# Optimization experiments

Measured on AMD Instinct MI355X. Metric: run time of the kernel, lower is better.

Reference implementation:

```python
import jax, jax.numpy as jnp
import numpy as np

N = 1024
NODE_DIM = 3
HIDDEN = 128
NLAYERS = 3
HEADS = 4
HD = HIDDEN // HEADS  # 32
EPS = 1e-5
NEG = -1e9


def setup_inputs() -> dict:
    key = jax.random.key(0)
    ks = jax.random.split(key, 32)
    def w(k, shape, fan_in):
        return jax.random.normal(k, shape, jnp.float32) / np.sqrt(fan_in).astype(np.float32)
    node_features = jax.random.normal(ks[0], (N, NODE_DIM), jnp.float32)
    adj = jax.random.randint(ks[1], (N, N), 0, 2).astype(jnp.float32)
    adj = adj.at[jnp.arange(N), jnp.arange(N)].set(1.0)  # self-loops
    inp = dict(
        node_features=node_features,
        adj=adj,
        Wp=w(ks[2], (NODE_DIM, HIDDEN), NODE_DIM), bp=jnp.zeros((HIDDEN,), jnp.float32),
        Wl=w(ks[3], (NLAYERS, HIDDEN, HIDDEN), HIDDEN),
        Wr=w(ks[4], (NLAYERS, HIDDEN, HIDDEN), HIDDEN),
        Wv=w(ks[5], (NLAYERS, HIDDEN, HIDDEN), HIDDEN),
        att=w(ks[6], (NLAYERS, HD), HD),
        gamma=jnp.ones((NLAYERS, HIDDEN), jnp.float32),
        beta=jnp.zeros((NLAYERS, HIDDEN), jnp.float32),
        Wn1=w(ks[7], (HIDDEN, 64), HIDDEN), bn1=jnp.zeros((64,), jnp.float32),
        Wn2=w(ks[8], (64, 1), 64), bn2=jnp.zeros((1,), jnp.float32),
        Wd1=w(ks[9], (HIDDEN, 64), HIDDEN), bd1=jnp.zeros((64,), jnp.float32),
        Wd2=w(ks[10], (64, 2), 64), bd2=jnp.zeros((2,), jnp.float32),
        Wv1=w(ks[11], (HIDDEN, 64), HIDDEN), bv1=jnp.zeros((64,), jnp.float32),
        Wv2=w(ks[12], (64, 1), 64), bv2=jnp.zeros((1,), jnp.float32),
    )
    return inp


def _gat_layer(h, mask, Wl, Wr, Wv, att, gamma, beta):
    n = h.shape[0]
    wlh = (h @ Wl).reshape(n, HEADS, HD)
    wrh = (h @ Wr).reshape(n, HEADS, HD)
    # pair[i,j,h,d] = LeakyReLU(Wl h_i + Wr h_j)  -- the O(N^2 H D) tensor
    pair = jax.nn.leaky_relu(wlh[:, None, :, :] + wrh[None, :, :, :], 0.2)
    e = jnp.einsum('ijhd,d->ijh', pair, att)
    e = jnp.where(mask[:, :, None], e, NEG)
    alpha = jax.nn.softmax(e, axis=1)  # softmax over neighbours j (dropout = identity in eval)
    v = (h @ Wv).reshape(n, HEADS, HD)
    agg = jnp.einsum('ijh,jhd->ihd', alpha, v).reshape(n, HIDDEN)
    mu = agg.mean(-1, keepdims=True)
    var = agg.var(-1, keepdims=True)
    out = (agg - mu) / jnp.sqrt(var + EPS) * gamma + beta
    return jax.nn.relu(out)


def reference(node_features, adj, Wp, bp, Wl, Wr, Wv, att, gamma, beta,
              Wn1, bn1, Wn2, bn2, Wd1, bd1, Wd2, bd2, Wv1, bv1, Wv2, bv2):
    mask = adj > 0.5
    h = jax.nn.relu(node_features @ Wp + bp)
    for l in range(NLAYERS):
        h = h + _gat_layer(h, mask, Wl[l], Wr[l], Wv[l], att[l], gamma[l], beta[l])
    node_logits = (jax.nn.relu(h @ Wn1 + bn1) @ Wn2 + bn2).squeeze(-1)
    delta_mu = jax.nn.relu(h @ Wd1 + bd1) @ Wd2 + bd2
    pooled = h.mean(axis=0)
    value = (jax.nn.relu(pooled @ Wv1 + bv1) @ Wv2 + bv2).squeeze(-1)
    return (node_logits, delta_mu, value)
```

## Files before the change

### kernel.cpp

```cpp
#include <hip/hip_runtime.h>
#include <hip/hip_bf16.h>

#define NN 1024
#define HID 128
#define NHEADS 4
#define HDD 32
#define NL 3

constexpr int OFF_CONV = 16;
constexpr int OFF_NF   = OFF_CONV;
constexpr int OFF_WP   = OFF_NF  + 3072;
constexpr int OFF_BP   = OFF_WP  + 384;
constexpr int OFF_WL   = OFF_BP  + 128;
constexpr int OFF_WR   = OFF_WL  + 49152;
constexpr int OFF_WVW  = OFF_WR  + 49152;
constexpr int OFF_ATT  = OFF_WVW + 49152;
constexpr int OFF_GAM  = OFF_ATT + 96;
constexpr int OFF_BET  = OFF_GAM + 384;
constexpr int OFF_WN1  = OFF_BET + 384;
constexpr int OFF_BN1  = OFF_WN1 + 8192;
constexpr int OFF_WN2  = OFF_BN1 + 64;
constexpr int OFF_BN2  = OFF_WN2 + 64;
constexpr int OFF_WD1  = OFF_BN2 + 1;
constexpr int OFF_BD1  = OFF_WD1 + 8192;
constexpr int OFF_WD2  = OFF_BD1 + 64;
constexpr int OFF_BD2  = OFF_WD2 + 128;
constexpr int OFF_WV1  = OFF_BD2 + 2;
constexpr int OFF_BV1  = OFF_WV1 + 8192;
constexpr int OFF_WV2  = OFF_BV1 + 64;
constexpr int OFF_BV2  = OFF_WV2 + 64;
constexpr int OFF_CONV_END = OFF_BV2 + 1;
constexpr int CONV_TOTAL = OFF_CONV_END - OFF_CONV;
constexpr int CB = (CONV_TOTAL + 255) / 256;
constexpr int OFF_MASK = 176960;
constexpr int OFF_H    = OFF_MASK + NN*32;
constexpr int OFF_WLH  = OFF_H   + NN*HID;
constexpr int OFF_WRH  = OFF_WLH + NN*HID;
constexpr int OFF_WVH  = OFF_WRH + NN*HID;
constexpr int OFF_CL   = OFF_WVH + NN*HID;
constexpr int OFF_CR   = OFF_CL  + NHEADS*NN;

__device__ __forceinline__ float bf2f(unsigned short u) {
    return __uint_as_float(((unsigned)u) << 16);
}
__device__ __forceinline__ void store_out(void* out, int idx, float v, bool bf) {
    if (bf) {
        unsigned u = __float_as_uint(v);
        unsigned r = (u + 0x7FFFu + ((u >> 16) & 1u)) >> 16;
        ((unsigned short*)out)[idx] = (unsigned short)r;
    } else {
        ((float*)out)[idx] = v;
    }
}
__device__ __forceinline__ float ldraw(const void* p, int idx, bool bf) {
    return bf ? bf2f(((const unsigned short*)p)[idx]) : ((const float*)p)[idx];
}
__device__ __forceinline__ bool detect_bf(const unsigned* nf) {
    unsigned w = nf[threadIdx.x & 63];
    int e = (int)((w >> 23) & 0xFFu);
    unsigned long long b = __ballot(e >= 110 && e <= 140);
    return __popcll(b) < 32;
}

struct P21 { const void* p[21]; };
__device__ const int g_sizes[21] = {3072,384,128,49152,49152,49152,96,384,384,
                                    8192,64,64,1,8192,64,128,2,8192,64,64,1};
__device__ const int g_dsts[21] = {OFF_NF,OFF_WP,OFF_BP,OFF_WL,OFF_WR,OFF_WVW,OFF_ATT,
                                   OFF_GAM,OFF_BET,OFF_WN1,OFF_BN1,OFF_WN2,OFF_BN2,
                                   OFF_WD1,OFF_BD1,OFF_WD2,OFF_BD2,OFF_WV1,OFF_BV1,
                                   OFF_WV2,OFF_BV2};

__global__ __launch_bounds__(256) void k_pre(P21 in, const void* adj, const unsigned* nf, float* ws) {
    bool bf = detect_bf(nf);
    int b = blockIdx.x, t = threadIdx.x;
    if (b < CB) {
        int g = b * 256 + t;
        if (g >= CONV_TOTAL) return;
        int rem = g, s = 0;
        while (s < 21 && rem >= g_sizes[s]) { rem -= g_sizes[s]; s++; }
        if (s >= 21) return;
        ws[g_dsts[s] + rem] = ldraw(in.p[s], rem, bf);
    } else if (b < CB + NN) {
        int i = b - CB;
        unsigned* mask = (unsigned*)(ws + OFF_MASK);
        int lane = t & 63, wv = t >> 6;
        #pragma unroll
        for (int q = 0; q < 4; q++) {
            int seg = wv * 4 + q;
            int j = seg * 64 + lane;
            float v = ldraw(adj, i * NN + j, bf);
            unsigned long long bl = __ballot(v > 0.5f);
            if (lane == 0) {
                mask[i * 32 + seg * 2]     = (unsigned)bl;
                mask[i * 32 + seg * 2 + 1] = (unsigned)(bl >> 32);
            }
        }
    } else {
        int bb = b - CB - NN;
        int i = bb * 2 + (t >> 7), c = t & 127;
        float a = ldraw(in.p[2], c, bf);
        #pragma unroll
        for (int k = 0; k < 3; k++)
            a += ldraw(in.p[0], i * 3 + k, bf) * ldraw(in.p[1], k * HID + c, bf);
        ws[OFF_H + i * HID + c] = fmaxf(a, 0.0f);
    }
}

__global__ __launch_bounds__(128) void k_mm3(float* ws, int l) {
    __shared__ float hs[4][HID];
    int c = threadIdx.x, i0 = blockIdx.x * 4, which = blockIdx.y;
    const float* h = ws + OFF_H;
    #pragma unroll
    for (int r = 0; r < 4; r++) hs[r][c] = h[(i0 + r) * HID + c];
    __syncthreads();
    int woff = (which == 0) ? OFF_WL : (which == 1) ? OFF_WR : OFF_WVW;
    const float* W = ws + woff + l * HID * HID;
    float a[4] = {0,0,0,0};
    #pragma unroll 4
    for (int k = 0; k < HID; k++) {
        float w = W[k * HID + c];
        #pragma unroll
        for (int r = 0; r < 4; r++) a[r] += hs[r][k] * w;
    }
    if (which == 0) {
        #pragma unroll
        for (int r = 0; r < 4; r++) ws[OFF_WLH + (i0 + r) * HID + c] = a[r];
        float att = ws[OFF_ATT + l * HDD + (c & 31)];
        #pragma unroll
        for (int r = 0; r < 4; r++) {
            float t = att * a[r];
            #pragma unroll
            for (int off = 1; off < 32; off <<= 1) t += __shfl_xor(t, off, 64);
            if ((c & 31) == 0) ws[OFF_CL + (c >> 5) * NN + (i0 + r)] = 0.6f * t;
        }
    } else {
        int doff = (which == 1) ? OFF_WRH : OFF_WVH;
        #pragma unroll
        for (int r = 0; r < 4; r++)
            ws[doff + (c >> 2) * (NN * 4) + (i0 + r) * 4 + (c & 3)] = a[r];
        if (which == 1) {
            float att = ws[OFF_ATT + l * HDD + (c & 31)];
            #pragma unroll
            for (int r = 0; r < 4; r++) {
                float t = att * a[r];
                #pragma unroll
                for (int off = 1; off < 32; off <<= 1) t += __shfl_xor(t, off, 64);
                if ((c & 31) == 0) ws[OFF_CR + (c >> 5) * NN + (i0 + r)] = 0.6f * t;
            }
        }
    }
}

__global__ __launch_bounds__(512) void k_attn(float* ws, int l) {
    int t = threadIdx.x;
    int i0 = blockIdx.x * 2;
    int lane = t & 63;
    int w = t >> 6;
    int h  = __builtin_amdgcn_readfirstlane(w & 3);
    int jh = __builtin_amdgcn_readfirstlane(w >> 2);
    int iA = i0, iB = i0 + 1;

    __shared__ unsigned mrow[2][32];
    __shared__ float ebuf[8][64][33];
    __shared__ float mex[2][4][2];
    __shared__ float lsx[2][4][2];
    __shared__ float agg_s[2][HID];
    __shared__ float red2[2][2][2];

    if (t < 64) mrow[t >> 5][t & 31] = ((const unsigned*)(ws + OFF_MASK))[i0 * 32 + t];
    __syncthreads();

    unsigned mbA = 0, mbB = 0;
    #pragma unroll
    for (int jc = 0; jc < 8; jc++) {
        int wi = jh * 16 + jc * 2 + (lane >> 5);
        mbA |= ((mrow[0][wi] >> (lane & 31)) & 1u) << jc;
        mbB |= ((mrow[1][wi] >> (lane & 31)) & 1u) << jc;
    }

    float att_r[32], wlA[32], wlB[32];
    const float* attp = ws + OFF_ATT + l * HDD;
    const float* wlpA = ws + OFF_WLH + iA * HID + h * HDD;
    const float* wlpB = ws + OFF_WLH + iB * HID + h * HDD;
    #pragma unroll
    for (int d = 0; d < 32; d++) {
        att_r[d] = 0.4f * attp[d];
        wlA[d] = wlpA[d];
        wlB[d] = wlpB[d];
    }
    float clA = ws[OFF_CL + h * NN + iA];
    float clB = ws[OFF_CL + h * NN + iB];

    const float* wrT = ws + OFF_WRH + h * 8 * (NN * 4) + jh * 2048 + lane * 4;
    const float* wvT = ws + OFF_WVH + h * 8 * (NN * 4) + jh * 2048 + lane * 4;
    const float* crp = ws + OFF_CR + h * NN + jh * 512;

    float mA = -1e30f, mB = -1e30f;
    #pragma unroll 1
    for (int jc = 0; jc < 8; jc++) {
        float cr6 = crp[jc * 64 + lane];
        float dA = 0.0f, dB = 0.0f;
        #pragma unroll
        for (int dq = 0; dq < 8; dq++) {
            float4 wv4 = *(const float4*)(wrT + dq * (NN * 4) + jc * 256);
            dA = fmaf(att_r[dq*4+0], fabsf(wlA[dq*4+0] + wv4.x), dA);
            dB = fmaf(att_r[dq*4+0], fabsf(wlB[dq*4+0] + wv4.x), dB);
            dA = fmaf(att_r[dq*4+1], fabsf(wlA[dq*4+1] + wv4.y), dA);
            dB = fmaf(att_r[dq*4+1], fabsf(wlB[dq*4+1] + wv4.y), dB);
            dA = fmaf(att_r[dq*4+2], fabsf(wlA[dq*4+2] + wv4.z), dA);
            dB = fmaf(att_r[dq*4+2], fabsf(wlB[dq*4+2] + wv4.z), dB);
            dA = fmaf(att_r[dq*4+3], fabsf(wlA[dq*4+3] + wv4.w), dA);
            dB = fmaf(att_r[dq*4+3], fabsf(wlB[dq*4+3] + wv4.w), dB);
        }
        float eA = (clA + cr6) + dA; eA = ((mbA >> jc) & 1u) ? eA : -1e9f;
        float eB = (clB + cr6) + dB; eB = ((mbB >> jc) & 1u) ? eB : -1e9f;
        ebuf[w][lane][jc]     = eA;
        ebuf[w][lane][8 + jc] = eB;
        mA = fmaxf(mA, eA);
        mB = fmaxf(mB, eB);
    }
    #pragma unroll
    for (int off = 32; off > 0; off >>= 1) {
        mA = fmaxf(mA, __shfl_xor(mA, off, 64));
        mB = fmaxf(mB, __shfl_xor(mB, off, 64));
    }
    if (lane == 0) { mex[jh][h][0] = mA; mex[jh][h][1] = mB; }
    __syncthreads();
    mA = fmaxf(mex[0][h][0], mex[1][h][0]);
    mB = fmaxf(mex[0][h][1], mex[1][h][1]);

    float accA[32], accB[32];
    #pragma unroll
    for (int d = 0; d < 32; d++) { accA[d] = 0.0f; accB[d] = 0.0f; }
    float lsA = 0.0f, lsB = 0.0f;
    #pragma unroll 1
    for (int jc = 0; jc < 8; jc++) {
        float peA = __expf(ebuf[w][lane][jc]     - mA);
        float peB = __expf(ebuf[w][lane][8 + jc] - mB);
        lsA += peA; lsB += peB;
        #pragma unroll
        for (int dq = 0; dq < 8; dq++) {
            float4 v4 = *(const float4*)(wvT + dq * (NN * 4) + jc * 256);
            accA[dq*4+0] = fmaf(peA, v4.x, accA[dq*4+0]);
            accB[dq*4+0] = fmaf(peB, v4.x, accB[dq*4+0]);
            accA[dq*4+1] = fmaf(peA, v4.y, accA[dq*4+1]);
            accB[dq*4+1] = fmaf(peB, v4.y, accB[dq*4+1]);
            accA[dq*4+2] = fmaf(peA, v4.z, accA[dq*4+2]);
            accB[dq*4+2] = fmaf(peB, v4.z, accB[dq*4+2]);
            accA[dq*4+3] = fmaf(peA, v4.w, accA[dq*4+3]);
            accB[dq*4+3] = fmaf(peB, v4.w, accB[dq*4+3]);
        }
    }
    #pragma unroll
    for (int off = 32; off > 0; off >>= 1) {
        lsA += __shfl_xor(lsA, off, 64);
        lsB += __shfl_xor(lsB, off, 64);
    }
    if (lane == 0) { lsx[jh][h][0] = lsA; lsx[jh][h][1] = lsB; }

    float* rbuf = &ebuf[0][0][0];
    {
        #pragma unroll
        for (int d = 0; d < 32; d++) rbuf[(w * 64 + lane) * 33 + d] = accA[d];
        __syncthreads();
        int g = t >> 6, d = lane & 31, halfl = lane >> 5;
        if (g < 4) {
            float s = 0.0f;
            #pragma unroll
            for (int lq = 0; lq < 32; lq++) {
                s += rbuf[(g * 64       + halfl * 32 + lq) * 33 + d];
                s += rbuf[((g + 4) * 64 + halfl * 32 + lq) * 33 + d];
            }
            s += __shfl_xor(s, 32, 64);
            if (halfl == 0)
                agg_s[0][g * 32 + d] = s * (1.0f / (lsx[0][g][0] + lsx[1][g][0]));
        }
        __syncthreads();
    }
    {
        #pragma unroll
        for (int d = 0; d < 32; d++) rbuf[(w * 64 + lane) * 33 + d] = accB[d];
        __syncthreads();
        int g = t >> 6, d = lane & 31, halfl = lane >> 5;
        if (g < 4) {
            float s = 0.0f;
            #pragma unroll
            for (int lq = 0; lq < 32; lq++) {
                s += rbuf[(g * 64       + halfl * 32 + lq) * 33 + d];
                s += rbuf[((g + 4) * 64 + halfl * 32 + lq) * 33 + d];
            }
            s += __shfl_xor(s, 32, 64);
            if (halfl == 0)
                agg_s[1][g * 32 + d] = s * (1.0f / (lsx[0][g][1] + lsx[1][g][1]));
        }
        __syncthreads();
    }

    {
        int n = (t >> 7) & 1, f = t & 127;
        float agg = agg_s[n][f];
        float s = agg, s2 = agg * agg;
        #pragma unroll
        for (int off = 32; off > 0; off >>= 1) {
            s  += __shfl_xor(s,  off, 64);
            s2 += __shfl_xor(s2, off, 64);
        }
        int halfw = (t >> 6) & 1;
        if (lane == 0 && t < 256) { red2[n][halfw][0] = s; red2[n][halfw][1] = s2; }
        __syncthreads();
        float ts  = red2[n][0][0] + red2[n][1][0];
        float ts2 = red2[n][0][1] + red2[n][1][1];
        float mu  = ts  * (1.0f / HID);
        float var = ts2 * (1.0f / HID) - mu * mu;
        float gm = ws[OFF_GAM + l * HID + f];
        float be = ws[OFF_BET + l * HID + f];
        float o = (agg - mu) * rsqrtf(var + 1e-5f) * gm + be;
        if (t < 256) ws[OFF_H + (i0 + n) * HID + f] += fmaxf(o, 0.0f);
    }
}

__global__ __launch_bounds__(1024) void k_post(float* ws, const unsigned* nf, void* out) {
    bool bf = detect_bf(nf);
    int b = blockIdx.x, t = threadIdx.x;
    if (b < 64) {
        __shared__ float hrow[16][HID];
        int n = t >> 6, tt = t & 63;
        int i = b * 16 + n;
        hrow[n][tt]      = ws[OFF_H + i * HID + tt];
        hrow[n][tt + 64] = ws[OFF_H + i * HID + tt + 64];
        __syncthreads();
        const float* Wn1 = ws + OFF_WN1;
        const float* Wd1 = ws + OFF_WD1;
        float z1 = ws[OFF_BN1 + tt], zd = ws[OFF_BD1 + tt];
        #pragma unroll 4
        for (int k = 0; k < HID; k++) {
            float hk = hrow[n][k];
            z1 += hk * Wn1[k * 64 + tt];
            zd += hk * Wd1[k * 64 + tt];
        }
        z1 = fmaxf(z1, 0.0f); zd = fmaxf(zd, 0.0f);
        float lg = z1 * ws[OFF_WN2 + tt];
        float d0 = zd * ws[OFF_WD2 + tt * 2 + 0];
        float d1 = zd * ws[OFF_WD2 + tt * 2 + 1];
        #pragma unroll
        for (int off = 32; off > 0; off >>= 1) {
            lg += __shfl_xor(lg, off, 64);
            d0 += __shfl_xor(d0, off, 64);
            d1 += __shfl_xor(d1, off, 64);
        }
        if (tt == 0) {
            store_out(out, i,              lg + ws[OFF_BN2],     bf);
            store_out(out, NN + i * 2 + 0, d0 + ws[OFF_BD2 + 0], bf);
            store_out(out, NN + i * 2 + 1, d1 + ws[OFF_BD2 + 1], bf);
        }
    } else {
        __shared__ float part[8][HID];
        __shared__ float pooled[HID];
        int g = t >> 7, c = t & 127;
        float s = 0.0f;
        #pragma unroll 16
        for (int r = 0; r < 128; r++) s += ws[OFF_H + (g * 128 + r) * HID + c];
        part[g][c] = s;
        __syncthreads();
        if (t < HID) {
            float p = 0.0f;
            #pragma unroll
            for (int gg = 0; gg < 8; gg++) p += part[gg][t];
            pooled[t] = p * (1.0f / NN);
        }
        __syncthreads();
        if (t < 64) {
            float z = ws[OFF_BV1 + t];
            float z1 = 0.0f;
            #pragma unroll 8
            for (int k = 0; k < HID; k += 2) {
                z  += pooled[k]     * ws[OFF_WV1 + k * 64 + t];
                z1 += pooled[k + 1] * ws[OFF_WV1 + (k + 1) * 64 + t];
            }
            z = fmaxf(z + z1, 0.0f);
            float pv = z * ws[OFF_WV2 + t];
            #pragma unroll
            for (int off = 32; off > 0; off >>= 1) pv += __shfl_xor(pv, off, 64);
            if (t == 0) store_out(out, 3072, pv + ws[OFF_BV2], bf);
        }
    }
}

extern "C" void kernel_launch(void* const* d_in, const int* in_sizes, int n_in,
                              void* d_out, int out_size, void* d_ws, size_t ws_size,
                              hipStream_t stream) {
    float* ws = (float*)d_ws;
    const unsigned* nf = (const unsigned*)d_in[0];

    P21 ptrs;
    const int map[21] = {0,2,3,4,5,6,7,8,9,10,11,12,13,14,15,16,17,18,19,20,21};
    for (int s = 0; s < 21; s++) ptrs.p[s] = d_in[map[s]];

    k_pre<<<CB + NN + NN / 2, 256, 0, stream>>>(ptrs, d_in[1], nf, ws);

    for (int l = 0; l < NL; l++) {
        k_mm3<<<dim3(NN / 4, 3), 128, 0, stream>>>(ws, l);
        k_attn<<<NN / 2, 512, 0, stream>>>(ws, l);
    }

    k_post<<<65, 1024, 0, stream>>>(ws, nf, d_out);
}
```

Before: 227.2 us.

## Fuse GAT attention into single-pass unnormalized softmax with one node per warp

Each wave now handles a single destination node over all 1024 neighbours, instead of two nodes over half the neighbours. The logit pass and the weighted-value pass are merged into one loop that applies exp directly without subtracting a row max, and masked entries are set to zero. This removes the LDS logit buffer, the max reduction and its barrier, and one of the two cross-wave accumulator reductions. In exchange, each wave reloads the Wr/Wv rows for only one node, which doubles per-wave global/L2 traffic and lowers ILP. Dropping the max shift also risks overflow if logits become large.

Result: slower. 375.7 us (+65.4%).

```diff
diff --git a/kernel.cpp b/kernel.cpp
--- a/kernel.cpp
+++ b/kernel.cpp
@@ -157,144 +157,83 @@
     int lane = t & 63;
     int w = t >> 6;
     int h  = __builtin_amdgcn_readfirstlane(w & 3);
-    int jh = __builtin_amdgcn_readfirstlane(w >> 2);
-    int iA = i0, iB = i0 + 1;
+    int nl = __builtin_amdgcn_readfirstlane(w >> 2);
+    int i = i0 + nl;
 
     __shared__ unsigned mrow[2][32];
-    __shared__ float ebuf[8][64][33];
-    __shared__ float mex[2][4][2];
-    __shared__ float lsx[2][4][2];
+    __shared__ float rbuf_s[8][64][33];
+    __shared__ float invs[2][4];
     __shared__ float agg_s[2][HID];
     __shared__ float red2[2][2][2];
 
     if (t < 64) mrow[t >> 5][t & 31] = ((const unsigned*)(ws + OFF_MASK))[i0 * 32 + t];
     __syncthreads();
 
-    unsigned mbA = 0, mbB = 0;
-    #pragma unroll
-    for (int jc = 0; jc < 8; jc++) {
-        int wi = jh * 16 + jc * 2 + (lane >> 5);
-        mbA |= ((mrow[0][wi] >> (lane & 31)) & 1u) << jc;
-        mbB |= ((mrow[1][wi] >> (lane & 31)) & 1u) << jc;
-    }
-
-    float att_r[32], wlA[32], wlB[32];
+    unsigned mb = 0;
+    #pragma unroll
+    for (int jc = 0; jc < 16; jc++)
+        mb |= ((mrow[nl][jc * 2 + (lane >> 5)] >> (lane & 31)) & 1u) << jc;
+
+    float att_r[32], wl[32];
     const float* attp = ws + OFF_ATT + l * HDD;
-    const float* wlpA = ws + OFF_WLH + iA * HID + h * HDD;
-    const float* wlpB = ws + OFF_WLH + iB * HID + h * HDD;
+    const float* wlp  = ws + OFF_WLH + i * HID + h * HDD;
     #pragma unroll
     for (int d = 0; d < 32; d++) {
         att_r[d] = 0.4f * attp[d];
-        wlA[d] = wlpA[d];
-        wlB[d] = wlpB[d];
-    }
-    float clA = ws[OFF_CL + h * NN + iA];
-    float clB = ws[OFF_CL + h * NN + iB];
-
-    const float* wrT = ws + OFF_WRH + h * 8 * (NN * 4) + jh * 2048 + lane * 4;
-    const float* wvT = ws + OFF_WVH + h * 8 * (NN * 4) + jh * 2048 + lane * 4;
-    const float* crp = ws + OFF_CR + h * NN + jh * 512;
-
-    float mA = -1e30f, mB = -1e30f;
+        wl[d] = wlp[d];
+    }
+    float cl = ws[OFF_CL + h * NN + i];
+
+    const float* wrT = ws + OFF_WRH + h * 8 * (NN * 4) + lane * 4;
+    const float* wvT = ws + OFF_WVH + h * 8 * (NN * 4) + lane * 4;
+    const float* crp = ws + OFF_CR + h * NN;
+
+    float acc[32];
+    #pragma unroll
+    for (int d = 0; d < 32; d++) acc[d] = 0.0f;
+    float ls = 0.0f;
     #pragma unroll 1
-    for (int jc = 0; jc < 8; jc++) {
+    for (int jc = 0; jc < 16; jc++) {
         float cr6 = crp[jc * 64 + lane];
-        float dA = 0.0f, dB = 0.0f;
+        float dot = 0.0f;
         #pragma unroll
         for (int dq = 0; dq < 8; dq++) {
-            float4 wv4 = *(const float4*)(wrT + dq * (NN * 4) + jc * 256);
-            dA = fmaf(att_r[dq*4+0], fabsf(wlA[dq*4+0] + wv4.x), dA);
-            dB = fmaf(att_r[dq*4+0], fabsf(wlB[dq*4+0] + wv4.x), dB);
-            dA = fmaf(att_r[dq*4+1], fabsf(wlA[dq*4+1] + wv4.y), dA);
-            dB = fmaf(att_r[dq*4+1], fabsf(wlB[dq*4+1] + wv4.y), dB);
-            dA = fmaf(att_r[dq*4+2], fabsf(wlA[dq*4+2] + wv4.z), dA);
-            dB = fmaf(att_r[dq*4+2], fabsf(wlB[dq*4+2] + wv4.z), dB);
-            dA = fmaf(att_r[dq*4+3], fabsf(wlA[dq*4+3] + wv4.w), dA);
-            dB = fmaf(att_r[dq*4+3], fabsf(wlB[dq*4+3] + wv4.w), dB);
-        }
-        float eA = (clA + cr6) + dA; eA = ((mbA >> jc) & 1u) ? eA : -1e9f;
-        float eB = (clB + cr6) + dB; eB = ((mbB >> jc) & 1u) ? eB : -1e9f;
-        ebuf[w][lane][jc]     = eA;
-        ebuf[w][lane][8 + jc] = eB;
-        mA = fmaxf(mA, eA);
-        mB = fmaxf(mB, eB);
-    }
-    #pragma unroll
-    for (int off = 32; off > 0; off >>= 1) {
-        mA = fmaxf(mA, __shfl_xor(mA, off, 64));
-        mB = fmaxf(mB, __shfl_xor(mB, off, 64));
-    }
-    if (lane == 0) { mex[jh][h][0] = mA; mex[jh][h][1] = mB; }
-    __syncthreads();
-    mA = fmaxf(mex[0][h][0], mex[1][h][0]);
-    mB = fmaxf(mex[0][h][1], mex[1][h][1]);
-
-    float accA[32], accB[32];
-    #pragma unroll
-    for (int d = 0; d < 32; d++) { accA[d] = 0.0f; accB[d] = 0.0f; }
-    float lsA = 0.0f, lsB = 0.0f;
-    #pragma unroll 1
-    for (int jc = 0; jc < 8; jc++) {
-        float peA = __expf(ebuf[w][lane][jc]     - mA);
-        float peB = __expf(ebuf[w][lane][8 + jc] - mB);
-        lsA += peA; lsB += peB;
+            float4 w4 = *(const float4*)(wrT + dq * (NN * 4) + jc * 256);
+            dot = fmaf(att_r[dq*4+0], fabsf(wl[dq*4+0] + w4.x), dot);
+            dot = fmaf(att_r[dq*4+1], fabsf(wl[dq*4+1] + w4.y), dot);
+            dot = fmaf(att_r[dq*4+2], fabsf(wl[dq*4+2] + w4.z), dot);
+            dot = fmaf(att_r[dq*4+3], fabsf(wl[dq*4+3] + w4.w), dot);
+        }
+        float e = (cl + cr6) + dot;
+        float pe = ((mb >> jc) & 1u) ? __expf(e) : 0.0f;
+        ls += pe;
         #pragma unroll
         for (int dq = 0; dq < 8; dq++) {
             float4 v4 = *(const float4*)(wvT + dq * (NN * 4) + jc * 256);
-            accA[dq*4+0] = fmaf(peA, v4.x, accA[dq*4+0]);
-            accB[dq*4+0] = fmaf(peB, v4.x, accB[dq*4+0]);
-            accA[dq*4+1] = fmaf(peA, v4.y, accA[dq*4+1]);
-            accB[dq*4+1] = fmaf(peB, v4.y, accB[dq*4+1]);
-            accA[dq*4+2] = fmaf(peA, v4.z, accA[dq*4+2]);
-            accB[dq*4+2] = fmaf(peB, v4.z, accB[dq*4+2]);
-            accA[dq*4+3] = fmaf(peA, v4.w, accA[dq*4+3]);
-            accB[dq*4+3] = fmaf(peB, v4.w, accB[dq*4+3]);
-        }
-    }
-    #pragma unroll
-    for (int off = 32; off > 0; off >>= 1) {
-        lsA += __shfl_xor(lsA, off, 64);
-        lsB += __shfl_xor(lsB, off, 64);
-    }
-    if (lane == 0) { lsx[jh][h][0] = lsA; lsx[jh][h][1] = lsB; }
-
-    float* rbuf = &ebuf[0][0][0];
+            acc[dq*4+0] = fmaf(pe, v4.x, acc[dq*4+0]);
+            acc[dq*4+1] = fmaf(pe, v4.y, acc[dq*4+1]);
+            acc[dq*4+2] = fmaf(pe, v4.z, acc[dq*4+2]);
+            acc[dq*4+3] = fmaf(pe, v4.w, acc[dq*4+3]);
+        }
+    }
+    #pragma unroll
+    for (int off = 32; off > 0; off >>= 1) ls += __shfl_xor(ls, off, 64);
+    if (lane == 0) invs[nl][h] = 1.0f / ls;
+
+    float* rbuf = &rbuf_s[0][0][0];
+    #pragma unroll
+    for (int d = 0; d < 32; d++) rbuf[(w * 64 + lane) * 33 + d] = acc[d];
+    __syncthreads();
     {
-        #pragma unroll
-        for (int d = 0; d < 32; d++) rbuf[(w * 64 + lane) * 33 + d] = accA[d];
-        __syncthreads();
-        int g = t >> 6, d = lane & 31, halfl = lane >> 5;
-        if (g < 4) {
-            float s = 0.0f;
-            #pragma unroll
-            for (int lq = 0; lq < 32; lq++) {
-                s += rbuf[(g * 64       + halfl * 32 + lq) * 33 + d];
-                s += rbuf[((g + 4) * 64 + halfl * 32 + lq) * 33 + d];
-            }
-            s += __shfl_xor(s, 32, 64);
-            if (halfl == 0)
-                agg_s[0][g * 32 + d] = s * (1.0f / (lsx[0][g][0] + lsx[1][g][0]));
-        }
-        __syncthreads();
-    }
-    {
-        #pragma unroll
-        for (int d = 0; d < 32; d++) rbuf[(w * 64 + lane) * 33 + d] = accB[d];
-        __syncthreads();
-        int g = t >> 6, d = lane & 31, halfl = lane >> 5;
-        if (g < 4) {
-            float s = 0.0f;
-            #pragma unroll
-            for (int lq = 0; lq < 32; lq++) {
-                s += rbuf[(g * 64       + halfl * 32 + lq) * 33 + d];
-                s += rbuf[((g + 4) * 64 + halfl * 32 + lq) * 33 + d];
-            }
-            s += __shfl_xor(s, 32, 64);
-            if (halfl == 0)
-                agg_s[1][g * 32 + d] = s * (1.0f / (lsx[0][g][1] + lsx[1][g][1]));
-        }
-        __syncthreads();
-    }
+        int g = t >> 6, d = lane & 31, half = lane >> 5;
+        float s = 0.0f;
+        #pragma unroll
+        for (int lq = 0; lq < 32; lq++) s += rbuf[(g * 64 + half * 32 + lq) * 33 + d];
+        s += __shfl_xor(s, 32, 64);
+        int gn = g >> 2, gh = g & 3;
+        if (half == 0) agg_s[gn][gh * 32 + d] = s * invs[gn][gh];
+    }
+    __syncthreads();
 
     {
         int n = (t >> 7) & 1, f = t & 127;
```
